# Kernel optimization log

Measured on AMD Instinct MI355X. Metric: run time of the kernel, lower is better.

Reference implementation:

```python
import jax, jax.numpy as jnp
import numpy as np

E = 8          # num experts
H = 1024       # hidden size
I = 512        # moe intermediate size
K = 2          # top_k
B, S = 1, 2048


def setup_inputs() -> dict:
    key = jax.random.key(0)
    k1, k2, k3, k4, k5 = jax.random.split(key, 5)
    hidden_states = jax.random.normal(k1, (B, S, H), dtype=jnp.float32)
    router_indices = jax.random.randint(k2, (B * S, K), 0, E, dtype=jnp.int64)
    routing_weights = jax.random.uniform(k3, (B * S, K), dtype=jnp.float32)
    # kaiming-uniform-ish init per expert
    bound_gu = 1.0 / np.sqrt(H)
    bound_d = 1.0 / np.sqrt(I)
    gate_up_proj = jax.random.uniform(k4, (E, H, 2 * I), dtype=jnp.float32,
                                      minval=-bound_gu, maxval=bound_gu)
    down_proj = jax.random.uniform(k5, (E, I, H), dtype=jnp.float32,
                                   minval=-bound_d, maxval=bound_d)
    return {
        "hidden_states": hidden_states,
        "router_indices": router_indices,
        "routing_weights": routing_weights,
        "gate_up_proj": gate_up_proj,
        "down_proj": down_proj,
    }


def reference(hidden_states, router_indices, routing_weights, gate_up_proj, down_proj):
    b, s, h = hidden_states.shape
    x = hidden_states.reshape(b * s, h)                    # [T, H]
    # combine weights: sum over top-k slots of routing weight for each expert
    one_hot = jax.nn.one_hot(router_indices, E, dtype=x.dtype)   # [T, K, E]
    combine = jnp.einsum('tke,tk->te', one_hot, routing_weights)  # [T, E]
    # dense dispatch: every token through every expert, masked/weighted by combine
    gate_up = jnp.einsum('th,ehf->tef', x, gate_up_proj)   # [T, E, 2I]
    gate, up = jnp.split(gate_up, 2, axis=-1)              # [T, E, I] each
    inter = jax.nn.silu(gate) * up                         # SwiGLU (no limit clamp)
    out = jnp.einsum('tef,efh,te->th', inter, down_proj, combine)  # [T, H]
    return out.reshape(b, s, h)
```

## Files before the change

kernel.cpp:

```cpp
#include <hip/hip_runtime.h>
#include <stdint.h>

#define T_TOK 2048
#define H_DIM 1024
#define ID    512
#define E_NUM 8
#define NPAIR 4096
#define BM    64
#define MAXTILES 72

typedef _Float16 half_t;
typedef _Float16 f16x8 __attribute__((ext_vector_type(8)));
typedef _Float16 f16x4 __attribute__((ext_vector_type(4)));
typedef float    f32x4 __attribute__((ext_vector_type(4)));

#define XB_OFF    ((size_t)0)
#define WGU_OFF   ((size_t)(4u << 20))
#define WDN_OFF   ((size_t)(20u << 20))
#define INTER_OFF ((size_t)(28u << 20))
#define META_OFF  ((size_t)(32u << 20))
#define PAIRW_OFF ((size_t)((32u << 20) + 32768))

__device__ __forceinline__ void gload_lds16(const void* g, void* l) {
    __builtin_amdgcn_global_load_lds(
        (const __attribute__((address_space(1))) unsigned int*)g,
        (__attribute__((address_space(3))) unsigned int*)l,
        16, 0, 0);
}

__device__ __forceinline__ void cvt_tile64(const float* __restrict__ in,
                                           half_t* __restrict__ out,
                                           int r0, int c0, int out_stride,
                                           char* smem) {
    float (*tile)[65] = (float(*)[65])smem;
    int tid = threadIdx.x;
#pragma unroll
    for (int it = 0; it < 4; it++) {
        int idx = tid + it * 256;
        int r = idx >> 4, c4 = (idx & 15) * 4;
        float4 v = *(const float4*)(in + (size_t)(r0 + r) * 1024 + c0 + c4);
        tile[r][c4] = v.x; tile[r][c4 + 1] = v.y; tile[r][c4 + 2] = v.z; tile[r][c4 + 3] = v.w;
    }
    __syncthreads();
#pragma unroll
    for (int it = 0; it < 4; it++) {
        int idx = tid + it * 256;
        int oc = idx >> 4, r4 = (idx & 15) * 4;
        f16x4 o;
        o[0] = (half_t)tile[r4][oc];
        o[1] = (half_t)tile[r4 + 1][oc];
        o[2] = (half_t)tile[r4 + 2][oc];
        o[3] = (half_t)tile[r4 + 3][oc];
        *(f16x4*)(out + (size_t)(c0 + oc) * out_stride + r0 + r4) = o;
    }
}

__global__ __launch_bounds__(256) void k_prep(const float* __restrict__ x,
                                              const int* __restrict__ ridx,
                                              const float* __restrict__ rw,
                                              const float* __restrict__ wgu,
                                              half_t* __restrict__ xb,
                                              half_t* __restrict__ wguT,
                                              int* __restrict__ meta,
                                              float* __restrict__ pair_w) {
    __shared__ char smem[16704];
    int b = blockIdx.x, tid = threadIdx.x;
    if (b < 1024) {
        int g = b * 256 + tid;
        size_t b0 = (size_t)g * 8;
        float4 v0 = *(const float4*)(x + b0);
        float4 v1 = *(const float4*)(x + b0 + 4);
        f16x8 o;
        o[0] = (half_t)v0.x; o[1] = (half_t)v0.y; o[2] = (half_t)v0.z; o[3] = (half_t)v0.w;
        o[4] = (half_t)v1.x; o[5] = (half_t)v1.y; o[6] = (half_t)v1.z; o[7] = (half_t)v1.w;
        *(f16x8*)(xb + b0) = o;
    } else if (b == 1024) {
        __shared__ int cnt[E_NUM], cur[E_NUM], base[E_NUM];
        if (tid < E_NUM) { cnt[tid] = 0; cur[tid] = 0; }
        __syncthreads();
        for (int i = tid; i < NPAIR; i += 256) atomicAdd(&cnt[ridx[i]], 1);
        __syncthreads();
        if (tid == 0) {
            int acc = 0, nt = 0;
            for (int e = 0; e < E_NUM; e++) {
                base[e] = acc;
                for (int r = 0; r < cnt[e]; r += BM) {
                    meta[8 + nt] = e; meta[88 + nt] = acc + r; meta[168 + nt] = acc + cnt[e]; nt++;
                }
                acc += cnt[e];
            }
            meta[0] = nt;
        }
        __syncthreads();
        for (int i = tid; i < NPAIR; i += 256) {
            int e = ridx[i];
            int pos = atomicAdd(&cur[e], 1);
            int slot = base[e] + pos;
            meta[256 + slot] = i >> 1;
            pair_w[slot] = rw[i];
        }
    } else {
        int t = b - 1025;
        int e = t >> 8, rem = t & 255;
        int h0 = (rem >> 4) * 64, f0 = (rem & 15) * 64;
        cvt_tile64(wgu + (size_t)e * 1024 * 1024, wguT + (size_t)e * 1024 * 1024,
                   h0, f0, 1024, smem);
    }
}

template <int MODE>
__global__ __launch_bounds__(256) void k_gemm(const int* __restrict__ meta,
                                              const half_t* __restrict__ amat,
                                              const half_t* __restrict__ wT,
                                              const float* __restrict__ pair_w,
                                              void* __restrict__ outp,
                                              const float* __restrict__ aux_in,
                                              half_t* __restrict__ aux_out,
                                              float4* __restrict__ zero_out) {
    constexpr int KSZ = MODE ? ID : H_DIM;
    constexpr int NKT = KSZ / 64;
    __shared__ char smem[49152];

    int d = blockIdx.x;
    if (MODE == 0 && d >= 576) {
        int d2 = d - 576;
        if (d2 < 1024) {
            int e = d2 >> 7, rem = d2 & 127;
            int h0 = (rem >> 3) * 64, i0 = (rem & 7) * 64;
            cvt_tile64(aux_in + (size_t)e * ID * 1024, aux_out + (size_t)e * 1024 * ID,
                       i0, h0, ID, smem);
        } else {
            int z = d2 - 1024;
            float4 zv = make_float4(0.f, 0.f, 0.f, 0.f);
            float4* p = zero_out + (size_t)z * 1024 + threadIdx.x;
            p[0] = zv; p[256] = zv; p[512] = zv; p[768] = zv;
        }
        return;
    }

    int l = (d & 7) * MAXTILES + (d >> 3);
    int bx = l >> 3, by = l & 7;
    int nt = meta[0];
    if (bx >= nt) return;
    int e = meta[8 + bx], row0 = meta[88 + bx], rend = meta[168 + bx];
    const int* pair_token = meta + 256;

    int tid = threadIdx.x, lane = tid & 63, wid = tid >> 6;

    const half_t* asrc[2]; int aoff[2];
#pragma unroll
    for (int i = 0; i < 2; i++) {
        int gch = wid * 2 + i, c = gch * 64 + lane;
        int r = c >> 3, pc = c & 7, lc = pc ^ (r & 7);
        int pr = row0 + r; if (pr > NPAIR - 1) pr = NPAIR - 1;
        const half_t* rowp = (MODE == 0) ? amat + (size_t)pair_token[pr] * KSZ
                                         : amat + (size_t)pr * KSZ;
        asrc[i] = rowp + lc * 8;
        aoff[i] = gch * 1024 + lane * 16;
    }
    const half_t* wbase = wT + (size_t)e * 1024 * KSZ;
    const half_t* bsrc[4]; int boff[4];
#pragma unroll
    for (int i = 0; i < 4; i++) {
        int gch = wid * 4 + i, c = gch * 64 + lane;
        int r = c >> 3, pc = c & 7, lc = pc ^ (r & 7);
        int physcol;
        if (MODE == 0) {
            int wn_r = r >> 5, fn_r = (r >> 4) & 1, ll = r & 15;
            physcol = by * 64 + wn_r * 16 + ll + (fn_r ? 512 : 0);
        } else {
            physcol = by * 128 + r;
        }
        bsrc[i] = wbase + (size_t)physcol * KSZ + lc * 8;
        boff[i] = gch * 1024 + lane * 16;
    }

#define STAGE(buf, kt)                                                             \
    {                                                                              \
        _Pragma("unroll")                                                          \
        for (int i = 0; i < 2; i++)                                                \
            gload_lds16(asrc[i] + (kt) * 64, smem + (buf) * 8192 + aoff[i]);       \
        _Pragma("unroll")                                                          \
        for (int i = 0; i < 4; i++)                                                \
            gload_lds16(bsrc[i] + (kt) * 64, smem + 16384 + (buf) * 16384 + boff[i]); \
    }

    f32x4 acc[4][2] = {};

    STAGE(0, 0);
    __syncthreads();

    for (int kt = 0; kt < NKT; kt++) {
        int cur = kt & 1;
        if (kt + 1 < NKT) STAGE(cur ^ 1, kt + 1);
        const char* Ab = smem + cur * 8192;
        const char* Bb = smem + 16384 + cur * 16384;
#pragma unroll
        for (int ks = 0; ks < 2; ks++) {
            f16x8 af[4], bf2[2];
#pragma unroll
            for (int f = 0; f < 4; f++) {
                int ar = f * 16 + (lane & 15);
                int apc = (ks * 4 + (lane >> 4)) ^ (ar & 7);
                af[f] = *(const f16x8*)(Ab + ar * 128 + apc * 16);
            }
#pragma unroll
            for (int f = 0; f < 2; f++) {
                int br = wid * 32 + f * 16 + (lane & 15);
                int bpc = (ks * 4 + (lane >> 4)) ^ (br & 7);
                bf2[f] = *(const f16x8*)(Bb + br * 128 + bpc * 16);
            }
#pragma unroll
            for (int fm = 0; fm < 4; fm++)
#pragma unroll
                for (int fn = 0; fn < 2; fn++)
                    acc[fm][fn] = __builtin_amdgcn_mfma_f32_16x16x32_f16(af[fm], bf2[fn], acc[fm][fn], 0, 0, 0);
        }
        __syncthreads();
    }

    if (MODE == 0) {
        half_t* inter = (half_t*)outp;
#pragma unroll
        for (int fm = 0; fm < 4; fm++) {
            int rbase = fm * 16 + (lane >> 4) * 4;
#pragma unroll
            for (int j = 0; j < 4; j++) {
                int packed = row0 + rbase + j;
                if (packed < rend) {
                    float gv = acc[fm][0][j], uv = acc[fm][1][j];
                    float s = gv / (1.0f + __expf(-gv)) * uv;
                    int col = by * 64 + wid * 16 + (lane & 15);
                    inter[(size_t)packed * ID + col] = (half_t)s;
                }
            }
        }
    } else {
        float* out = (float*)outp;
#pragma unroll
        for (int fm = 0; fm < 4; fm++) {
            int rbase = fm * 16 + (lane >> 4) * 4;
#pragma unroll
            for (int j = 0; j < 4; j++) {
                int packed = row0 + rbase + j;
                if (packed < rend) {
                    int t = pair_token[packed];
                    float pw = pair_w[packed];
#pragma unroll
                    for (int fn = 0; fn < 2; fn++) {
                        int col = by * 128 + wid * 32 + fn * 16 + (lane & 15);
                        __hip_atomic_fetch_add(&out[(size_t)t * H_DIM + col],
                                               acc[fm][fn][j] * pw,
                                               __ATOMIC_RELAXED,
                                               __HIP_MEMORY_SCOPE_AGENT);
                    }
                }
            }
        }
    }
#undef STAGE
}

extern "C" void kernel_launch(void* const* d_in, const int* in_sizes, int n_in,
                              void* d_out, int out_size, void* d_ws, size_t ws_size,
                              hipStream_t stream) {
    const float* x    = (const float*)d_in[0];
    const int*   ridx = (const int*)d_in[1];
    const float* rw   = (const float*)d_in[2];
    const float* wgu  = (const float*)d_in[3];
    const float* wdn  = (const float*)d_in[4];
    float* out = (float*)d_out;

    char* ws = (char*)d_ws;
    half_t* xb    = (half_t*)(ws + XB_OFF);
    half_t* wguT  = (half_t*)(ws + WGU_OFF);
    half_t* wdnT  = (half_t*)(ws + WDN_OFF);
    half_t* inter = (half_t*)(ws + INTER_OFF);
    int*    meta  = (int*)(ws + META_OFF);
    float*  pair_w = (float*)(ws + PAIRW_OFF);

    k_prep<<<3073, 256, 0, stream>>>(x, ridx, rw, wgu, xb, wguT, meta, pair_w);
    k_gemm<0><<<2112, 256, 0, stream>>>(meta, xb, wguT, pair_w, inter, wdn, wdnT, (float4*)out);
    k_gemm<1><<<576, 256, 0, stream>>>(meta, inter, wdnT, pair_w, out, nullptr, nullptr, nullptr);
}
```

Baseline: 64.61 us.

## Use 2-wave blocks with larger per-wave tiles and 3-stage LDS pipeline

The grouped GEMM kernels now run 128-thread blocks (2 waves) that each compute a 64x64 sub-tile, doubling per-wave MFMA work and register accumulators. The double-buffered K loop becomes a triple-buffered pipeline using explicit vmcnt waits and raw barriers, so loads run two stages ahead and one barrier is issued per iteration. The transpose and zero-fill side paths are adapted to 128 threads. This trades occupancy and LDS (72KB per block) for better latency hiding and data reuse per wave.

```diff
diff --git a/kernel.cpp b/kernel.cpp
--- a/kernel.cpp
+++ b/kernel.cpp
@@ -28,6 +28,7 @@
         16, 0, 0);
 }
 
+template <int NT>
 __device__ __forceinline__ void cvt_tile64(const float* __restrict__ in,
                                            half_t* __restrict__ out,
                                            int r0, int c0, int out_stride,
@@ -35,16 +36,16 @@
     float (*tile)[65] = (float(*)[65])smem;
     int tid = threadIdx.x;
 #pragma unroll
-    for (int it = 0; it < 4; it++) {
-        int idx = tid + it * 256;
+    for (int it = 0; it < 1024 / NT; it++) {
+        int idx = tid + it * NT;
         int r = idx >> 4, c4 = (idx & 15) * 4;
         float4 v = *(const float4*)(in + (size_t)(r0 + r) * 1024 + c0 + c4);
         tile[r][c4] = v.x; tile[r][c4 + 1] = v.y; tile[r][c4 + 2] = v.z; tile[r][c4 + 3] = v.w;
     }
     __syncthreads();
 #pragma unroll
-    for (int it = 0; it < 4; it++) {
-        int idx = tid + it * 256;
+    for (int it = 0; it < 1024 / NT; it++) {
+        int idx = tid + it * NT;
         int oc = idx >> 4, r4 = (idx & 15) * 4;
         f16x4 o;
         o[0] = (half_t)tile[r4][oc];
@@ -103,13 +104,13 @@
         int t = b - 1025;
         int e = t >> 8, rem = t & 255;
         int h0 = (rem >> 4) * 64, f0 = (rem & 15) * 64;
-        cvt_tile64(wgu + (size_t)e * 1024 * 1024, wguT + (size_t)e * 1024 * 1024,
-                   h0, f0, 1024, smem);
+        cvt_tile64<256>(wgu + (size_t)e * 1024 * 1024, wguT + (size_t)e * 1024 * 1024,
+                        h0, f0, 1024, smem);
     }
 }
 
 template <int MODE>
-__global__ __launch_bounds__(256) void k_gemm(const int* __restrict__ meta,
+__global__ __launch_bounds__(128) void k_gemm(const int* __restrict__ meta,
                                               const half_t* __restrict__ amat,
                                               const half_t* __restrict__ wT,
                                               const float* __restrict__ pair_w,
@@ -119,7 +120,7 @@
                                               float4* __restrict__ zero_out) {
     constexpr int KSZ = MODE ? ID : H_DIM;
     constexpr int NKT = KSZ / 64;
-    __shared__ char smem[49152];
+    __shared__ __align__(16) char smem[73728];
 
     int d = blockIdx.x;
     if (MODE == 0 && d >= 576) {
@@ -127,13 +128,14 @@
         if (d2 < 1024) {
             int e = d2 >> 7, rem = d2 & 127;
             int h0 = (rem >> 3) * 64, i0 = (rem & 7) * 64;
-            cvt_tile64(aux_in + (size_t)e * ID * 1024, aux_out + (size_t)e * 1024 * ID,
-                       i0, h0, ID, smem);
+            cvt_tile64<128>(aux_in + (size_t)e * ID * 1024, aux_out + (size_t)e * 1024 * ID,
+                            i0, h0, ID, smem);
         } else {
             int z = d2 - 1024;
             float4 zv = make_float4(0.f, 0.f, 0.f, 0.f);
             float4* p = zero_out + (size_t)z * 1024 + threadIdx.x;
-            p[0] = zv; p[256] = zv; p[512] = zv; p[768] = zv;
+#pragma unroll
+            for (int k = 0; k < 8; k++) p[k * 128] = zv;
         }
         return;
     }
@@ -147,11 +149,11 @@
 
     int tid = threadIdx.x, lane = tid & 63, wid = tid >> 6;
 
-    const half_t* asrc[2]; int aoff[2];
-#pragma unroll
-    for (int i = 0; i < 2; i++) {
-        int gch = wid * 2 + i, c = gch * 64 + lane;
-        int r = c >> 3, pc = c & 7, lc = pc ^ (r & 7);
+    const half_t* asrc[4]; int aoff[4];
+#pragma unroll
+    for (int i = 0; i < 4; i++) {
+        int gch = wid * 4 + i;
+        int r = gch * 8 + (lane >> 3), pc = lane & 7, lc = pc ^ (r & 7);
         int pr = row0 + r; if (pr > NPAIR - 1) pr = NPAIR - 1;
         const half_t* rowp = (MODE == 0) ? amat + (size_t)pair_token[pr] * KSZ
                                          : amat + (size_t)pr * KSZ;
@@ -159,65 +161,73 @@
         aoff[i] = gch * 1024 + lane * 16;
     }
     const half_t* wbase = wT + (size_t)e * 1024 * KSZ;
-    const half_t* bsrc[4]; int boff[4];
-#pragma unroll
-    for (int i = 0; i < 4; i++) {
-        int gch = wid * 4 + i, c = gch * 64 + lane;
-        int r = c >> 3, pc = c & 7, lc = pc ^ (r & 7);
+    const half_t* bsrc[8]; int boff[8];
+#pragma unroll
+    for (int i = 0; i < 8; i++) {
+        int gch = wid * 8 + i;
+        int br = gch * 8 + (lane >> 3), pc = lane & 7, lc = pc ^ (br & 7);
         int physcol;
         if (MODE == 0) {
-            int wn_r = r >> 5, fn_r = (r >> 4) & 1, ll = r & 15;
-            physcol = by * 64 + wn_r * 16 + ll + (fn_r ? 512 : 0);
+            int w = br >> 6, f = (br >> 4) & 3, ll = br & 15;
+            physcol = by * 64 + w * 32 + (f & 1) * 16 + ll + ((f & 2) ? 512 : 0);
         } else {
-            physcol = by * 128 + r;
+            physcol = by * 128 + br;
         }
         bsrc[i] = wbase + (size_t)physcol * KSZ + lc * 8;
-        boff[i] = gch * 1024 + lane * 16;
-    }
-
-#define STAGE(buf, kt)                                                             \
-    {                                                                              \
-        _Pragma("unroll")                                                          \
-        for (int i = 0; i < 2; i++)                                                \
-            gload_lds16(asrc[i] + (kt) * 64, smem + (buf) * 8192 + aoff[i]);       \
-        _Pragma("unroll")                                                          \
-        for (int i = 0; i < 4; i++)                                                \
-            gload_lds16(bsrc[i] + (kt) * 64, smem + 16384 + (buf) * 16384 + boff[i]); \
-    }
-
-    f32x4 acc[4][2] = {};
-
-    STAGE(0, 0);
-    __syncthreads();
-
-    for (int kt = 0; kt < NKT; kt++) {
-        int cur = kt & 1;
-        if (kt + 1 < NKT) STAGE(cur ^ 1, kt + 1);
-        const char* Ab = smem + cur * 8192;
-        const char* Bb = smem + 16384 + cur * 16384;
+        boff[i] = 8192 + gch * 1024 + lane * 16;
+    }
+
+    auto stage = [&](int bufb, int kt) {
+        char* base = smem + bufb * 24576;
+#pragma unroll
+        for (int i = 0; i < 4; i++) gload_lds16(asrc[i] + kt * 64, base + aoff[i]);
+#pragma unroll
+        for (int i = 0; i < 8; i++) gload_lds16(bsrc[i] + kt * 64, base + boff[i]);
+    };
+
+    f32x4 acc[4][4] = {};
+
+    auto compute = [&](int bufb) {
+        const char* Ab = smem + bufb * 24576;
+        const char* Bb = Ab + 8192;
 #pragma unroll
         for (int ks = 0; ks < 2; ks++) {
-            f16x8 af[4], bf2[2];
+            f16x8 af[4], bf[4];
 #pragma unroll
             for (int f = 0; f < 4; f++) {
                 int ar = f * 16 + (lane & 15);
                 int apc = (ks * 4 + (lane >> 4)) ^ (ar & 7);
                 af[f] = *(const f16x8*)(Ab + ar * 128 + apc * 16);
-            }
-#pragma unroll
-            for (int f = 0; f < 2; f++) {
-                int br = wid * 32 + f * 16 + (lane & 15);
+                int br = wid * 64 + f * 16 + (lane & 15);
                 int bpc = (ks * 4 + (lane >> 4)) ^ (br & 7);
-                bf2[f] = *(const f16x8*)(Bb + br * 128 + bpc * 16);
+                bf[f] = *(const f16x8*)(Bb + br * 128 + bpc * 16);
             }
 #pragma unroll
             for (int fm = 0; fm < 4; fm++)
 #pragma unroll
-                for (int fn = 0; fn < 2; fn++)
-                    acc[fm][fn] = __builtin_amdgcn_mfma_f32_16x16x32_f16(af[fm], bf2[fn], acc[fm][fn], 0, 0, 0);
-        }
-        __syncthreads();
-    }
+                for (int fn = 0; fn < 4; fn++)
+                    acc[fm][fn] = __builtin_amdgcn_mfma_f32_16x16x32_f16(af[fm], bf[fn], acc[fm][fn], 0, 0, 0);
+        }
+    };
+
+    stage(0, 0);
+    stage(1, 1);
+    int cur = 0, stg = 2;
+    for (int kt = 0; kt < NKT - 2; kt++) {
+        asm volatile("s_waitcnt vmcnt(12)" ::: "memory");
+        __builtin_amdgcn_s_barrier();
+        stage(stg, kt + 2);
+        compute(cur);
+        cur = cur == 2 ? 0 : cur + 1;
+        stg = stg == 2 ? 0 : stg + 1;
+    }
+    asm volatile("s_waitcnt vmcnt(12)" ::: "memory");
+    __builtin_amdgcn_s_barrier();
+    compute(cur);
+    cur = cur == 2 ? 0 : cur + 1;
+    asm volatile("s_waitcnt vmcnt(0)" ::: "memory");
+    __builtin_amdgcn_s_barrier();
+    compute(cur);
 
     if (MODE == 0) {
         half_t* inter = (half_t*)outp;
@@ -228,10 +238,12 @@
             for (int j = 0; j < 4; j++) {
                 int packed = row0 + rbase + j;
                 if (packed < rend) {
-                    float gv = acc[fm][0][j], uv = acc[fm][1][j];
-                    float s = gv / (1.0f + __expf(-gv)) * uv;
-                    int col = by * 64 + wid * 16 + (lane & 15);
-                    inter[(size_t)packed * ID + col] = (half_t)s;
+                    int col = by * 64 + wid * 32 + (lane & 15);
+                    float g0 = acc[fm][0][j], u0 = acc[fm][2][j];
+                    float g1 = acc[fm][1][j], u1 = acc[fm][3][j];
+                    half_t* rowp = inter + (size_t)packed * ID;
+                    rowp[col]      = (half_t)(g0 / (1.0f + __expf(-g0)) * u0);
+                    rowp[col + 16] = (half_t)(g1 / (1.0f + __expf(-g1)) * u1);
                 }
             }
         }
@@ -247,8 +259,8 @@
                     int t = pair_token[packed];
                     float pw = pair_w[packed];
 #pragma unroll
-                    for (int fn = 0; fn < 2; fn++) {
-                        int col = by * 128 + wid * 32 + fn * 16 + (lane & 15);
+                    for (int fn = 0; fn < 4; fn++) {
+                        int col = by * 128 + wid * 64 + fn * 16 + (lane & 15);
                         __hip_atomic_fetch_add(&out[(size_t)t * H_DIM + col],
                                                acc[fm][fn][j] * pw,
                                                __ATOMIC_RELAXED,
@@ -258,7 +270,6 @@
             }
         }
     }
-#undef STAGE
 }
 
 extern "C" void kernel_launch(void* const* d_in, const int* in_sizes, int n_in,
@@ -280,6 +291,6 @@
     float*  pair_w = (float*)(ws + PAIRW_OFF);
 
     k_prep<<<3073, 256, 0, stream>>>(x, ridx, rw, wgu, xb, wguT, meta, pair_w);
-    k_gemm<0><<<2112, 256, 0, stream>>>(meta, xb, wguT, pair_w, inter, wdn, wdnT, (float4*)out);
-    k_gemm<1><<<576, 256, 0, stream>>>(meta, inter, wdnT, pair_w, out, nullptr, nullptr, nullptr);
-}
+    k_gemm<0><<<2112, 128, 0, stream>>>(meta, xb, wguT, pair_w, inter, wdn, wdnT, (float4*)out);
+    k_gemm<1><<<576, 128, 0, stream>>>(meta, inter, wdnT, pair_w, out, nullptr, nullptr, nullptr);
+}
```

Measured after the change: 86.01 us. 33.1% more time.

## Split down-projection GEMM along K and move output zeroing into prep kernel

Applied to the files above, without the earlier changes.

The down-projection GEMM now splits its K dimension (512) into two halves. Each expert tile therefore launches twice as many blocks (1152 instead of 576), and the partial results are presumably accumulated atomically into the output. Zeroing of the output buffer moves from the gate/up GEMM kernel into the prep kernel, which shrinks the first GEMM launch. The goal is more parallelism in the small second GEMM, at the cost of extra atomic traffic and a shorter K loop per block.

```diff
diff --git a/kernel.cpp b/kernel.cpp
--- a/kernel.cpp
+++ b/kernel.cpp
@@ -28,6 +28,7 @@
         16, 0, 0);
 }
 
+template <int NT>
 __device__ __forceinline__ void cvt_tile64(const float* __restrict__ in,
                                            half_t* __restrict__ out,
                                            int r0, int c0, int out_stride,
@@ -35,16 +36,16 @@
     float (*tile)[65] = (float(*)[65])smem;
     int tid = threadIdx.x;
 #pragma unroll
-    for (int it = 0; it < 4; it++) {
-        int idx = tid + it * 256;
+    for (int it = 0; it < 1024 / NT; it++) {
+        int idx = tid + it * NT;
         int r = idx >> 4, c4 = (idx & 15) * 4;
         float4 v = *(const float4*)(in + (size_t)(r0 + r) * 1024 + c0 + c4);
         tile[r][c4] = v.x; tile[r][c4 + 1] = v.y; tile[r][c4 + 2] = v.z; tile[r][c4 + 3] = v.w;
     }
     __syncthreads();
 #pragma unroll
-    for (int it = 0; it < 4; it++) {
-        int idx = tid + it * 256;
+    for (int it = 0; it < 1024 / NT; it++) {
+        int idx = tid + it * NT;
         int oc = idx >> 4, r4 = (idx & 15) * 4;
         f16x4 o;
         o[0] = (half_t)tile[r4][oc];
@@ -62,7 +63,8 @@
                                               half_t* __restrict__ xb,
                                               half_t* __restrict__ wguT,
                                               int* __restrict__ meta,
-                                              float* __restrict__ pair_w) {
+                                              float* __restrict__ pair_w,
+                                              float4* __restrict__ zero_out) {
     __shared__ char smem[16704];
     int b = blockIdx.x, tid = threadIdx.x;
     if (b < 1024) {
@@ -99,12 +101,17 @@
             meta[256 + slot] = i >> 1;
             pair_w[slot] = rw[i];
         }
-    } else {
+    } else if (b < 3073) {
         int t = b - 1025;
         int e = t >> 8, rem = t & 255;
         int h0 = (rem >> 4) * 64, f0 = (rem & 15) * 64;
-        cvt_tile64(wgu + (size_t)e * 1024 * 1024, wguT + (size_t)e * 1024 * 1024,
-                   h0, f0, 1024, smem);
+        cvt_tile64<256>(wgu + (size_t)e * 1024 * 1024, wguT + (size_t)e * 1024 * 1024,
+                        h0, f0, 1024, smem);
+    } else {
+        int z = b - 3073;
+        float4 zv = make_float4(0.f, 0.f, 0.f, 0.f);
+        float4* p = zero_out + (size_t)z * 1024 + tid;
+        p[0] = zv; p[256] = zv; p[512] = zv; p[768] = zv;
     }
 }
 
@@ -115,35 +122,34 @@
                                               const float* __restrict__ pair_w,
                                               void* __restrict__ outp,
                                               const float* __restrict__ aux_in,
-                                              half_t* __restrict__ aux_out,
-                                              float4* __restrict__ zero_out) {
+                                              half_t* __restrict__ aux_out) {
     constexpr int KSZ = MODE ? ID : H_DIM;
-    constexpr int NKT = KSZ / 64;
-    __shared__ char smem[49152];
+    constexpr int NKT = MODE ? 4 : 16;
+    __shared__ __align__(16) char smem[49152];
 
     int d = blockIdx.x;
     if (MODE == 0 && d >= 576) {
         int d2 = d - 576;
-        if (d2 < 1024) {
-            int e = d2 >> 7, rem = d2 & 127;
-            int h0 = (rem >> 3) * 64, i0 = (rem & 7) * 64;
-            cvt_tile64(aux_in + (size_t)e * ID * 1024, aux_out + (size_t)e * 1024 * ID,
-                       i0, h0, ID, smem);
-        } else {
-            int z = d2 - 1024;
-            float4 zv = make_float4(0.f, 0.f, 0.f, 0.f);
-            float4* p = zero_out + (size_t)z * 1024 + threadIdx.x;
-            p[0] = zv; p[256] = zv; p[512] = zv; p[768] = zv;
-        }
+        int e = d2 >> 7, rem = d2 & 127;
+        int h0 = (rem >> 3) * 64, i0 = (rem & 7) * 64;
+        cvt_tile64<256>(aux_in + (size_t)e * ID * 1024, aux_out + (size_t)e * 1024 * ID,
+                        i0, h0, ID, smem);
         return;
     }
 
-    int l = (d & 7) * MAXTILES + (d >> 3);
-    int bx = l >> 3, by = l & 7;
+    int bx, by, kz;
+    if (MODE == 0) {
+        int l = (d & 7) * 72 + (d >> 3);
+        bx = l >> 3; by = l & 7; kz = 0;
+    } else {
+        int l = (d & 7) * 144 + (d >> 3);
+        bx = l >> 4; by = (l >> 1) & 7; kz = l & 1;
+    }
     int nt = meta[0];
     if (bx >= nt) return;
     int e = meta[8 + bx], row0 = meta[88 + bx], rend = meta[168 + bx];
     const int* pair_token = meta + 256;
+    int k0 = kz * 256;
 
     int tid = threadIdx.x, lane = tid & 63, wid = tid >> 6;
 
@@ -155,7 +161,7 @@
         int pr = row0 + r; if (pr > NPAIR - 1) pr = NPAIR - 1;
         const half_t* rowp = (MODE == 0) ? amat + (size_t)pair_token[pr] * KSZ
                                          : amat + (size_t)pr * KSZ;
-        asrc[i] = rowp + lc * 8;
+        asrc[i] = rowp + k0 + lc * 8;
         aoff[i] = gch * 1024 + lane * 16;
     }
     const half_t* wbase = wT + (size_t)e * 1024 * KSZ;
@@ -171,7 +177,7 @@
         } else {
             physcol = by * 128 + r;
         }
-        bsrc[i] = wbase + (size_t)physcol * KSZ + lc * 8;
+        bsrc[i] = wbase + (size_t)physcol * KSZ + k0 + lc * 8;
         boff[i] = gch * 1024 + lane * 16;
     }
 
@@ -279,7 +285,7 @@
     int*    meta  = (int*)(ws + META_OFF);
     float*  pair_w = (float*)(ws + PAIRW_OFF);
 
-    k_prep<<<3073, 256, 0, stream>>>(x, ridx, rw, wgu, xb, wguT, meta, pair_w);
-    k_gemm<0><<<2112, 256, 0, stream>>>(meta, xb, wguT, pair_w, inter, wdn, wdnT, (float4*)out);
-    k_gemm<1><<<576, 256, 0, stream>>>(meta, inter, wdnT, pair_w, out, nullptr, nullptr, nullptr);
-}
+    k_prep<<<3585, 256, 0, stream>>>(x, ridx, rw, wgu, xb, wguT, meta, pair_w, (float4*)out);
+    k_gemm<0><<<1600, 256, 0, stream>>>(meta, xb, wguT, pair_w, inter, wdn, wdnT);
+    k_gemm<1><<<1152, 256, 0, stream>>>(meta, inter, wdnT, pair_w, out, nullptr, nullptr);
+}
```

After: 81.42 us. +26.0%, slower.
